# Optimization experiments

Hardware: AMD Instinct MI355X
Metric: run time of the kernel (lower is better)

The kernel has to match this reference:

```python
import jax, jax.numpy as jnp
import numpy as np

B, IN, H = 4096, 1024, 1024
G = 5  # i, f, o, c_hat, s gates

def setup_inputs() -> dict:
    key = jax.random.key(0)
    ks = jax.random.split(key, 24)
    s_in = 1.0 / np.sqrt(IN)
    s_h = 1.0 / np.sqrt(H)
    s_cat = 1.0 / np.sqrt(IN + H)
    inp = {
        'x': jax.random.normal(ks[0], (B, IN), jnp.float32),
        'h_prev': jax.random.normal(ks[1], (B, H), jnp.float32),
        'c_prev': jax.random.normal(ks[2], (B, H), jnp.float32),
        'ssg_state': jax.random.normal(ks[3], (B, H), jnp.float32),
        # stacked gate weights, torch Linear convention y = x @ W.T + b
        'Wx': jax.random.uniform(ks[4], (G, H, IN), jnp.float32, -s_in, s_in),
        'bWx': jax.random.uniform(ks[5], (G, H), jnp.float32, -s_in, s_in),
        'Ux': jax.random.uniform(ks[6], (G, H, H), jnp.float32, -s_h, s_h),
        'bUx': jax.random.uniform(ks[7], (G, H), jnp.float32, -s_h, s_h),
        # alpha MLP: Linear(IN+H -> H), ReLU, Linear(H -> 1), Sigmoid
        'a1_w': jax.random.uniform(ks[8], (H, IN + H), jnp.float32, -s_cat, s_cat),
        'a1_b': jax.random.uniform(ks[9], (H,), jnp.float32, -s_cat, s_cat),
        'a2_w': jax.random.uniform(ks[10], (1, H), jnp.float32, -s_h, s_h),
        'a2_b': jax.random.uniform(ks[11], (1,), jnp.float32, -s_h, s_h),
        'r1_w': jax.random.uniform(ks[12], (H, H), jnp.float32, -s_h, s_h),
        'r1_b': jax.random.uniform(ks[13], (H,), jnp.float32, -s_h, s_h),
        'r2_w': jax.random.uniform(ks[14], (H, H), jnp.float32, -s_h, s_h),
        'r2_b': jax.random.uniform(ks[15], (H,), jnp.float32, -s_h, s_h),
        'r3_w': jax.random.uniform(ks[16], (H, H), jnp.float32, -s_h, s_h),
        'r3_b': jax.random.uniform(ks[17], (H,), jnp.float32, -s_h, s_h),
        'ssg_w': jax.random.uniform(ks[18], (H, H), jnp.float32, -s_h, s_h),
        'ssg_b': jax.random.uniform(ks[19], (H,), jnp.float32, -s_h, s_h),
    }
    return inp


def reference(x, h_prev, c_prev, ssg_state, Wx, bWx, Ux, bUx,
              a1_w, a1_b, a2_w, a2_b, r1_w, r1_b, r2_w, r2_b, r3_w, r3_b,
              ssg_w, ssg_b):
    # all 5 gate pre-activations in two batched GEMMs: [G, B, H]
    g = (jnp.einsum('bi,ghi->gbh', x, Wx) + bWx[:, None, :]
         + jnp.einsum('bh,gkh->gbk', h_prev, Ux) + bUx[:, None, :])
    i_t = jax.nn.sigmoid(g[0])
    f_t = jax.nn.sigmoid(g[1])
    o_t = jax.nn.sigmoid(g[2])
    c_hat_t = jnp.tanh(g[3])
    s_t = jax.nn.sigmoid(g[4])  # computed as in original (unused when ssg_state given)

    combined = jnp.concatenate([x, h_prev], axis=-1)  # [B, IN+H]
    a_hidden = jax.nn.relu(combined @ a1_w.T + a1_b)
    alpha_t = jax.nn.sigmoid(a_hidden @ a2_w.T + a2_b)  # [B, 1]

    ssg_new = (ssg_state + h_prev) @ ssg_w.T + ssg_b  # ssg_state is not None branch

    c_t = f_t * c_prev + i_t * c_hat_t * s_t * alpha_t * ssg_new

    r = jax.nn.relu(h_prev @ r1_w.T + r1_b)
    r = jax.nn.relu(r @ r2_w.T + r2_b)
    residual = r @ r3_w.T + r3_b

    c_t = c_t + residual
    h_t = o_t * jnp.tanh(c_t)
    return (h_t, c_t, ssg_new)
```

## Files before the change

kernel.cpp:

```cpp
#include <hip/hip_runtime.h>
#include <hip/hip_bf16.h>

#define B_DIM 4096
#define H_DIM 1024
#define K1    2048
#define N1    6144

typedef __attribute__((ext_vector_type(8))) short bf16x8;
typedef __attribute__((ext_vector_type(4))) float f32x4;

__device__ __forceinline__ unsigned short f2bf(float f) {
  unsigned int x = __float_as_uint(f);
  x += 0x7fffu + ((x >> 16) & 1u);
  return (unsigned short)(x >> 16);
}
__device__ __forceinline__ float bf2f(unsigned short u) {
  return __uint_as_float(((unsigned int)u) << 16);
}
__device__ __forceinline__ float fast_sigmoid(float x) {
  return __builtin_amdgcn_rcpf(1.0f + __expf(-x));
}
__device__ __forceinline__ float fast_tanh(float x) {
  return 1.0f - 2.0f * __builtin_amdgcn_rcpf(1.0f + __expf(2.0f * x));
}
__device__ __forceinline__ void gload_lds16(const void* g, void* l) {
  __builtin_amdgcn_global_load_lds(
      (const __attribute__((address_space(1))) void*)g,
      (__attribute__((address_space(3))) void*)l, 16, 0, 0);
}

__device__ __forceinline__ int swz1k(int x) {
  return x ^ (((x >> 9) & 1) << 5);
}

__global__ __launch_bounds__(256) void prep_kernel(
    const float* __restrict__ x, const float* __restrict__ h,
    const float* __restrict__ ssg_state,
    const float* __restrict__ Wx, const float* __restrict__ Ux,
    const float* __restrict__ a1_w,
    const float* __restrict__ ssg_w, const float* __restrict__ r1_w,
    const float* __restrict__ r2_w, const float* __restrict__ r3_w,
    unsigned short* __restrict__ combined,
    unsigned short* __restrict__ ssg_in,
    unsigned short* __restrict__ W1,
    unsigned short* __restrict__ W2,
    unsigned short* __restrict__ W3,
    unsigned short* __restrict__ W4)
{
  const size_t NV0 = (size_t)B_DIM * K1 / 4;
  const size_t NV1 = (size_t)B_DIM * H_DIM / 4;
  const size_t NV3 = (size_t)N1 * K1 / 4;
  const size_t NV4 = (size_t)2048 * H_DIM / 4;
  const size_t NV5 = (size_t)H_DIM * H_DIM / 4;
  const size_t total = NV0 + NV1 + NV3 + NV4 + NV5 + NV5;
  const size_t stride = (size_t)gridDim.x * blockDim.x;

  for (size_t v = (size_t)blockIdx.x * blockDim.x + threadIdx.x; v < total; v += stride) {
    size_t idx = v;
    const float* src;
    unsigned short* dst;
    if (idx < NV0) {
      size_t e = idx * 4, b = e >> 11, k = e & 2047;
      src = (k < 1024) ? &x[(b << 10) + k] : &h[(b << 10) + (k - 1024)];
      dst = &combined[e];
    } else if ((idx -= NV0) < NV1) {
      size_t e = idx * 4;
      float4 a = *(const float4*)&ssg_state[e];
      float4 c = *(const float4*)&h[e];
      ushort4 o;
      o.x = f2bf(a.x + c.x); o.y = f2bf(a.y + c.y);
      o.z = f2bf(a.z + c.z); o.w = f2bf(a.w + c.w);
      *(ushort4*)&ssg_in[e] = o;
      continue;
    } else if ((idx -= NV1) < NV3) {
      size_t e = idx * 4, n = e >> 11, k = e & 2047;
      if (n < 5120) src = (k < 1024) ? &Wx[(n << 10) + k] : &Ux[(n << 10) + (k - 1024)];
      else          src = &a1_w[((n - 5120) << 11) + k];
      dst = &W1[e];
    } else if ((idx -= NV3) < NV4) {
      size_t e = idx * 4, n = e >> 10, k = e & 1023;
      src = (n < 1024) ? &ssg_w[(n << 10) + k] : &r1_w[((n - 1024) << 10) + k];
      dst = &W2[e];
    } else if ((idx -= NV4) < NV5) {
      size_t e = idx * 4; src = &r2_w[e]; dst = &W3[e];
    } else {
      idx -= NV5;
      size_t e = idx * 4; src = &r3_w[e]; dst = &W4[e];
    }
    float4 a = *(const float4*)src;
    ushort4 o;
    o.x = f2bf(a.x); o.y = f2bf(a.y); o.z = f2bf(a.z); o.w = f2bf(a.w);
    *(ushort4*)dst = o;
  }
}

__device__ __forceinline__ void body192(
    unsigned short* lds, const int bid,
    const unsigned short* __restrict__ A,
    const unsigned short* __restrict__ W,
    const float* __restrict__ bWx, const float* __restrict__ bUx,
    const float* __restrict__ a1_b,
    unsigned short* __restrict__ gates,
    unsigned short* __restrict__ a_hidden)
{
  constexpr int NT  = 32;
  constexpr int NTN = 32;
  constexpr int NWG = 32 * NTN;

  const int tid  = threadIdx.x;
  const int wave = tid >> 6;
  const int lane = tid & 63;
  const int wm = wave >> 1;
  const int wn = wave & 1;

  const int swz = (bid & 7) * (NWG / 8) + (bid >> 3);
  const int tm = swz / NTN, tn = swz % NTN;
  const int tmB = tm * 128, tnB = tn * 192;

  const int sidx = swz1k(lane * 16);
  const int r_l  = sidx >> 6;
  const int kel  = (sidx & 63) >> 1;
  const unsigned short* pA[2][2];
  const unsigned short* pB[3][2];
#pragma unroll
  for (int rg = 0; rg < 2; ++rg)
#pragma unroll
    for (int j = 0; j < 2; ++j)
      pA[rg][j] = A + (size_t)(tmB + (wave * 2 + rg) * 16 + r_l) * K1 + j * 32 + kel;
#pragma unroll
  for (int rg = 0; rg < 3; ++rg)
#pragma unroll
    for (int j = 0; j < 2; ++j)
      pB[rg][j] = W + (size_t)(tnB + (wave * 3 + rg) * 16 + r_l) * K1 + j * 32 + kel;

#define STAGE_A(tt) do { const int p_ = (tt) & 1;                                \
    _Pragma("unroll")                                                            \
    for (int rg = 0; rg < 2; ++rg)                                               \
      _Pragma("unroll")                                                          \
      for (int j = 0; j < 2; ++j)                                                \
        gload_lds16(pA[rg][j] + (size_t)(tt) * 64,                               \
                    &lds[p_ * 20480 + ((wave * 2 + rg) * 2 + j) * 512]);         \
  } while (0)
#define STAGE_B(tt) do { const int p_ = (tt) & 1;                                \
    _Pragma("unroll")                                                            \
    for (int rg = 0; rg < 3; ++rg)                                               \
      _Pragma("unroll")                                                          \
      for (int j = 0; j < 2; ++j)                                                \
        gload_lds16(pB[rg][j] + (size_t)(tt) * 64,                               \
                    &lds[p_ * 20480 + 8192 + ((wave * 3 + rg) * 2 + j) * 512]);  \
  } while (0)

  const int loc = swz1k((lane & 15) * 64 + (lane >> 4) * 16);

  f32x4 acc[4][6];
#pragma unroll
  for (int m = 0; m < 4; ++m)
#pragma unroll
    for (int n = 0; n < 6; ++n) acc[m][n] = (f32x4){0.f, 0.f, 0.f, 0.f};

  STAGE_A(0); STAGE_B(0);

#define MFMA24(aV, bV) do {                                                      \
    _Pragma("unroll")                                                            \
    for (int n = 0; n < 6; ++n) {                                                \
      _Pragma("unroll")                                                          \
      for (int m = 0; m < 4; ++m)                                                \
        acc[m][n] = __builtin_amdgcn_mfma_f32_16x16x32_bf16(                     \
            aV[m], bV[n], acc[m][n], 0, 0, 0);                                   \
    } } while (0)

  const char* lchar = (const char*)lds;
  for (int t = 0; t < NT; ++t) {
    asm volatile("s_waitcnt vmcnt(0)" ::: "memory");
    __builtin_amdgcn_s_barrier();

    const char* base = lchar + (t & 1) * 40960;
    const char* bA = base + wm * 8192 + loc;
    const char* bB = base + 16384 + wn * 12288 + loc;

    bf16x8 a0[4], a1[4], b0[6], b1[6];
#pragma unroll
    for (int n = 0; n < 6; ++n) b0[n] = *(const bf16x8*)(bB + (2 * n + 0) * 1024);
#pragma unroll
    for (int m = 0; m < 4; ++m) a0[m] = *(const bf16x8*)(bA + (2 * m + 0) * 1024);
    if (t + 1 < NT) STAGE_A(t + 1);
#pragma unroll
    for (int n = 0; n < 6; ++n) b1[n] = *(const bf16x8*)(bB + (2 * n + 1) * 1024);
#pragma unroll
    for (int m = 0; m < 4; ++m) a1[m] = *(const bf16x8*)(bA + (2 * m + 1) * 1024);
    if (t + 1 < NT) STAGE_B(t + 1);

    __builtin_amdgcn_s_setprio(1);
    MFMA24(a0, b0);
    __builtin_amdgcn_s_setprio(0);
    __builtin_amdgcn_s_setprio(1);
    MFMA24(a1, b1);
    __builtin_amdgcn_s_setprio(0);
  }
#undef MFMA24
#undef STAGE_A
#undef STAGE_B

  unsigned short* slab = &lds[wave * 1536];
  const int l15 = lane & 15, lq4 = (lane >> 4) << 2;
  const int colg0 = tnB + wn * 96;
  const int rowg0 = tmB + wm * 64;
  const size_t BH = (size_t)B_DIM * H_DIM;

  float biasv[6];
  int amode[6];
#pragma unroll
  for (int fn = 0; fn < 6; ++fn) {
    const int c = colg0 + fn * 16 + l15;
    if (c < 5120) {
      biasv[fn] = bWx[c] + bUx[c];
      amode[fn] = ((c >> 10) == 3) ? 1 : 0;
    } else {
      biasv[fn] = a1_b[c - 5120];
      amode[fn] = 2;
    }
  }
  __builtin_amdgcn_s_barrier();
#pragma unroll
  for (int fm = 0; fm < 4; ++fm) {
#pragma unroll
    for (int fn = 0; fn < 6; ++fn) {
      f32x4 v = acc[fm][fn];
#pragma unroll
      for (int j = 0; j < 4; ++j) {
        const int row = lq4 + j;
        const float xv = v[j] + biasv[fn];
        const float res = (amode[fn] == 1) ? fast_tanh(xv)
                         : (amode[fn] == 0) ? fast_sigmoid(xv)
                         : fmaxf(xv, 0.f);
        const int byte = (row * 192 + (fn * 16 + l15) * 2) ^ (((row >> 2) & 1) << 5);
        slab[byte >> 1] = f2bf(res);
      }
    }
    asm volatile("s_waitcnt lgkmcnt(0)" ::: "memory");
    __builtin_amdgcn_sched_barrier(0);
#pragma unroll
    for (int p = 0; p < 3; ++p) {
      const int id = p * 64 + lane;
      const int row = id / 12, cc = id - row * 12;
      const int byte = (row * 192 + cc * 16) ^ (((row >> 2) & 1) << 5);
      bf16x8 pk = *(const bf16x8*)((const char*)slab + byte);
      const int col = colg0 + cc * 8;
      const size_t r = (size_t)(rowg0 + fm * 16 + row);
      unsigned short* dst;
      if (col < 5120) dst = gates + (size_t)(col >> 10) * BH + r * 1024 + (col & 1023);
      else            dst = a_hidden + r * 1024 + (col - 5120);
      *(bf16x8*)dst = pk;
    }
    asm volatile("s_waitcnt lgkmcnt(0)" ::: "memory");
    __builtin_amdgcn_sched_barrier(0);
  }
}

template <int NT, int MODE>
__device__ __forceinline__ void gemm_body(
    unsigned short* lds, const int bid,
    const unsigned short* __restrict__ A0,
    const unsigned short* __restrict__ A1,
    const unsigned short* __restrict__ W,
    const float* __restrict__ b0, const float* __restrict__ b1,
    void* __restrict__ out0, void* __restrict__ out1)
{
  constexpr int KDIM = NT * 64;
  constexpr int NTN  = 16;
  constexpr int NWG  = 32 * NTN;

  const int tid  = threadIdx.x;
  const int wave = tid >> 6;
  const int lane = tid & 63;
  const int wm = wave >> 1;
  const int wn = wave & 1;

  const int swz = (bid & 7) * (NWG / 8) + (bid >> 3);
  const int tm = swz / NTN, tn = swz % NTN;
  const int tmB = tm * 128, tnB = tn * 128;

  const unsigned short* Abase = A0;
  int lda = 1024;
  if (tn >= 8) { Abase = A1; lda = 2048; }

  const int sidx = swz1k(lane * 16);
  const int r_l  = sidx >> 6;
  const int kel  = (sidx & 63) >> 1;
  const unsigned short* pA[2][2];
  const unsigned short* pB[2][2];
#pragma unroll
  for (int rg = 0; rg < 2; ++rg)
#pragma unroll
    for (int j = 0; j < 2; ++j) {
      const int rr = wave * 32 + rg * 16 + r_l;
      const int kk0 = j * 32 + kel;
      pA[rg][j] = Abase + (size_t)(tmB + rr) * lda + kk0;
      pB[rg][j] = W + (size_t)(tnB + rr) * KDIM + kk0;
    }

#define STAGE_A(tt) do { const int p_ = (tt) & 1;                                \
    _Pragma("unroll")                                                            \
    for (int rg = 0; rg < 2; ++rg)                                               \
      _Pragma("unroll")                                                          \
      for (int j = 0; j < 2; ++j)                                                \
        gload_lds16(pA[rg][j] + (size_t)(tt) * 64,                               \
                    &lds[p_ * 16384 + ((wave * 2 + rg) * 2 + j) * 512]);         \
  } while (0)
#define STAGE_B(tt) do { const int p_ = (tt) & 1;                                \
    _Pragma("unroll")                                                            \
    for (int rg = 0; rg < 2; ++rg)                                               \
      _Pragma("unroll")                                                          \
      for (int j = 0; j < 2; ++j)                                                \
        gload_lds16(pB[rg][j] + (size_t)(tt) * 64,                               \
                    &lds[p_ * 16384 + 8192 + ((wave * 2 + rg) * 2 + j) * 512]);  \
  } while (0)

  const int loc = swz1k((lane & 15) * 64 + (lane >> 4) * 16);

  f32x4 acc[4][4];
#pragma unroll
  for (int m = 0; m < 4; ++m)
#pragma unroll
    for (int n = 0; n < 4; ++n) acc[m][n] = (f32x4){0.f, 0.f, 0.f, 0.f};

  STAGE_A(0); STAGE_B(0);

#define MFMA16(aV, bV) do {                                                      \
    _Pragma("unroll")                                                            \
    for (int n = 0; n < 4; ++n) {                                                \
      _Pragma("unroll")                                                          \
      for (int m = 0; m < 4; ++m)                                                \
        acc[m][n] = __builtin_amdgcn_mfma_f32_16x16x32_bf16(                     \
            aV[m], bV[n], acc[m][n], 0, 0, 0);                                   \
    } } while (0)

  const char* lchar = (const char*)lds;
  for (int t = 0; t < NT; ++t) {
    asm volatile("s_waitcnt vmcnt(0)" ::: "memory");
    __builtin_amdgcn_s_barrier();

    const char* base = lchar + (t & 1) * 32768;
    const char* bA = base + wm * 8192 + loc;
    const char* bB = base + 16384 + wn * 8192 + loc;

    bf16x8 a0[4], a1[4], b0v[4], b1v[4];
#pragma unroll
    for (int n = 0; n < 4; ++n) b0v[n] = *(const bf16x8*)(bB + (2 * n + 0) * 1024);
#pragma unroll
    for (int m = 0; m < 4; ++m) a0[m] = *(const bf16x8*)(bA + (2 * m + 0) * 1024);
    if (t + 1 < NT) STAGE_A(t + 1);
#pragma unroll
    for (int n = 0; n < 4; ++n) b1v[n] = *(const bf16x8*)(bB + (2 * n + 1) * 1024);
#pragma unroll
    for (int m = 0; m < 4; ++m) a1[m] = *(const bf16x8*)(bA + (2 * m + 1) * 1024);
    if (t + 1 < NT) STAGE_B(t + 1);

    __builtin_amdgcn_s_setprio(1);
    MFMA16(a0, b0v);
    __builtin_amdgcn_s_setprio(0);
    __builtin_amdgcn_s_setprio(1);
    MFMA16(a1, b1v);
    __builtin_amdgcn_s_setprio(0);
  }
#undef MFMA16
#undef STAGE_A
#undef STAGE_B

  const int l15 = lane & 15, lq4 = (lane >> 4) << 2;
  const int rowg0 = tmB + wm * 64;

  if (tn < 8) {
    const int col0 = tn * 128 + wn * 64;
#pragma unroll
    for (int fn = 0; fn < 4; ++fn) {
      const int col = col0 + fn * 16 + l15;
      const float bias = b0[col];
#pragma unroll
      for (int fm = 0; fm < 4; ++fm) {
        f32x4 v = acc[fm][fn];
#pragma unroll
        for (int j = 0; j < 4; ++j) {
          const int r = rowg0 + fm * 16 + lq4 + j;
          ((float*)out0)[(size_t)r * 1024 + col] = v[j] + bias;
        }
      }
    }
    return;
  }

  unsigned short* slab = &lds[wave * 1024];
  const int lr8 = lane >> 3, lc8 = lane & 7;
  const int colg0 = (tn - 8) * 128 + wn * 64;
  unsigned short* outbase = (unsigned short*)out1;
  float biasv[4];
#pragma unroll
  for (int fn = 0; fn < 4; ++fn) biasv[fn] = b1[colg0 + fn * 16 + l15];
  __builtin_amdgcn_s_barrier();
#pragma unroll
  for (int fm = 0; fm < 4; ++fm) {
#pragma unroll
    for (int fn = 0; fn < 4; ++fn) {
      f32x4 v = acc[fm][fn];
#pragma unroll
      for (int j = 0; j < 4; ++j) {
        const int row = lq4 + j;
        const float res = fmaxf(v[j] + biasv[fn], 0.f);
        const int colb = ((fn * 16 + l15) * 2) ^ (((row >> 2) & 3) << 5);
        slab[(row * 128 + colb) >> 1] = f2bf(res);
      }
    }
    asm volatile("s_waitcnt lgkmcnt(0)" ::: "memory");
    __builtin_amdgcn_sched_barrier(0);
#pragma unroll
    for (int rd = 0; rd < 2; ++rd) {
      const int row = rd * 8 + lr8;
      const int cb = (lc8 * 16) ^ (((row >> 2) & 3) << 5);
      bf16x8 pk = *(const bf16x8*)((const char*)slab + row * 128 + cb);
      const size_t r = (size_t)(rowg0 + fm * 16 + row);
      *(bf16x8*)&outbase[r * 1024 + colg0 + lc8 * 8] = pk;
    }
    asm volatile("s_waitcnt lgkmcnt(0)" ::: "memory");
    __builtin_amdgcn_sched_barrier(0);
  }
}

__global__ __launch_bounds__(256, 2) void gemm_big(
    const unsigned short* __restrict__ combined,
    const unsigned short* __restrict__ ssg_in,
    const unsigned short* __restrict__ W1,
    const unsigned short* __restrict__ W2,
    const float* __restrict__ bWx, const float* __restrict__ bUx,
    const float* __restrict__ a1_b,
    const float* __restrict__ ssg_b, const float* __restrict__ r1_b,
    unsigned short* __restrict__ gates,
    unsigned short* __restrict__ a_hidden,
    float* __restrict__ ssg_out,
    unsigned short* __restrict__ r1)
{
  __shared__ unsigned short lds[40960];
  const int bid = blockIdx.x;
  if (bid < 1024) {
    body192(lds, bid, combined, W1, bWx, bUx, a1_b, gates, a_hidden);
  } else {
    gemm_body<16, 1>(lds, bid - 1024, ssg_in, combined + 1024, W2,
                     ssg_b, r1_b, ssg_out, r1);
  }
}

template <int MODE>
__global__ __launch_bounds__(256, 3) void gemm_small64(
    const unsigned short* __restrict__ A,
    const unsigned short* __restrict__ W,
    const float* __restrict__ bias,
    void* __restrict__ out)
{
  __shared__ unsigned short lds[24576];
  constexpr int NT = 16;

  const int tid  = threadIdx.x;
  const int wave = tid >> 6;
  const int lane = tid & 63;
  const int wm = wave >> 1;
  const int wn = wave & 1;

  const int bid = blockIdx.x;
  const int swz = (bid & 7) * 64 + (bid >> 3);
  const int tm = swz >> 3, tn = swz & 7;
  const int tmB = tm * 64, tnB = tn * 128;

  const int sidx = swz1k(lane * 16);
  const int r_l  = sidx >> 6;
  const int kel  = (sidx & 63) >> 1;
  const unsigned short* pA[2];
  const unsigned short* pB[2][2];
#pragma unroll
  for (int j = 0; j < 2; ++j)
    pA[j] = A + (size_t)(tmB + wave * 16 + r_l) * 1024 + j * 32 + kel;
#pragma unroll
  for (int rg = 0; rg < 2; ++rg)
#pragma unroll
    for (int j = 0; j < 2; ++j)
      pB[rg][j] = W + (size_t)(tnB + (wave * 2 + rg) * 16 + r_l) * 1024 + j * 32 + kel;

#define STAGE_A(tt) do { const int p_ = (tt) & 1;                                \
    _Pragma("unroll")                                                            \
    for (int j = 0; j < 2; ++j)                                                  \
      gload_lds16(pA[j] + (size_t)(tt) * 64,                                     \
                  &lds[p_ * 12288 + (wave * 2 + j) * 512]);                      \
  } while (0)
#define STAGE_B(tt) do { const int p_ = (tt) & 1;                                \
    _Pragma("unroll")                                                            \
    for (int rg = 0; rg < 2; ++rg)                                               \
      _Pragma("unroll")                                                          \
      for (int j = 0; j < 2; ++j)                                                \
        gload_lds16(pB[rg][j] + (size_t)(tt) * 64,                               \
                    &lds[p_ * 12288 + 4096 + ((wave * 2 + rg) * 2 + j) * 512]);  \
  } while (0)

  const int loc = swz1k((lane & 15) * 64 + (lane >> 4) * 16);

  f32x4 acc[2][4];
#pragma unroll
  for (int m = 0; m < 2; ++m)
#pragma unroll
    for (int n = 0; n < 4; ++n) acc[m][n] = (f32x4){0.f, 0.f, 0.f, 0.f};

  STAGE_A(0); STAGE_B(0);

  const char* lchar = (const char*)lds;
  for (int t = 0; t < NT; ++t) {
    asm volatile("s_waitcnt vmcnt(0)" ::: "memory");
    __builtin_amdgcn_s_barrier();

    const char* base = lchar + (t & 1) * 24576;
    const char* bA = base + wm * 4096 + loc;
    const char* bB = base + 8192 + wn * 8192 + loc;

    bf16x8 a0[2], a1[2], b0[4], b1[4];
#pragma unroll
    for (int n = 0; n < 4; ++n) b0[n] = *(const bf16x8*)(bB + (2 * n + 0) * 1024);
#pragma unroll
    for (int m = 0; m < 2; ++m) a0[m] = *(const bf16x8*)(bA + (2 * m + 0) * 1024);
    if (t + 1 < NT) STAGE_A(t + 1);
#pragma unroll
    for (int n = 0; n < 4; ++n) b1[n] = *(const bf16x8*)(bB + (2 * n + 1) * 1024);
#pragma unroll
    for (int m = 0; m < 2; ++m) a1[m] = *(const bf16x8*)(bA + (2 * m + 1) * 1024);
    if (t + 1 < NT) STAGE_B(t + 1);

    __builtin_amdgcn_s_setprio(1);
#pragma unroll
    for (int n = 0; n < 4; ++n)
#pragma unroll
      for (int m = 0; m < 2; ++m)
        acc[m][n] = __builtin_amdgcn_mfma_f32_16x16x32_bf16(a0[m], b0[n], acc[m][n], 0, 0, 0);
    __builtin_amdgcn_s_setprio(0);
    __builtin_amdgcn_s_setprio(1);
#pragma unroll
    for (int n = 0; n < 4; ++n)
#pragma unroll
      for (int m = 0; m < 2; ++m)
        acc[m][n] = __builtin_amdgcn_mfma_f32_16x16x32_bf16(a1[m], b1[n], acc[m][n], 0, 0, 0);
    __builtin_amdgcn_s_setprio(0);
  }
#undef STAGE_A
#undef STAGE_B

  const int l15 = lane & 15, lq4 = (lane >> 4) << 2;
  const int rowg0 = tmB + wm * 32;

  if (MODE == 3) {
    const int col0 = tnB + wn * 64;
#pragma unroll
    for (int fn = 0; fn < 4; ++fn) {
      const int col = col0 + fn * 16 + l15;
      const float bv = bias[col];
#pragma unroll
      for (int fm = 0; fm < 2; ++fm) {
        f32x4 v = acc[fm][fn];
#pragma unroll
        for (int j = 0; j < 4; ++j) {
          const int r = rowg0 + fm * 16 + lq4 + j;
          ((float*)out)[(size_t)r * 1024 + col] = v[j] + bv;
        }
      }
    }
    return;
  }

  unsigned short* slab = &lds[wave * 1024];
  const int lr8 = lane >> 3, lc8 = lane & 7;
  const int colg0 = tnB + wn * 64;
  unsigned short* outbase = (unsigned short*)out;
  float biasv[4];
#pragma unroll
  for (int fn = 0; fn < 4; ++fn) biasv[fn] = bias[colg0 + fn * 16 + l15];
  __builtin_amdgcn_s_barrier();
#pragma unroll
  for (int fm = 0; fm < 2; ++fm) {
#pragma unroll
    for (int fn = 0; fn < 4; ++fn) {
      f32x4 v = acc[fm][fn];
#pragma unroll
      for (int j = 0; j < 4; ++j) {
        const int row = lq4 + j;
        const float res = fmaxf(v[j] + biasv[fn], 0.f);
        const int colb = ((fn * 16 + l15) * 2) ^ (((row >> 2) & 3) << 5);
        slab[(row * 128 + colb) >> 1] = f2bf(res);
      }
    }
    asm volatile("s_waitcnt lgkmcnt(0)" ::: "memory");
    __builtin_amdgcn_sched_barrier(0);
#pragma unroll
    for (int rd = 0; rd < 2; ++rd) {
      const int row = rd * 8 + lr8;
      const int cb = (lc8 * 16) ^ (((row >> 2) & 3) << 5);
      bf16x8 pk = *(const bf16x8*)((const char*)slab + row * 128 + cb);
      const size_t r = (size_t)(rowg0 + fm * 16 + row);
      *(bf16x8*)&outbase[r * 1024 + colg0 + lc8 * 8] = pk;
    }
    asm volatile("s_waitcnt lgkmcnt(0)" ::: "memory");
    __builtin_amdgcn_sched_barrier(0);
  }
}

__global__ __launch_bounds__(256) void final_fused(
    const unsigned short* __restrict__ gates,
    const float* __restrict__ c_prev,
    const unsigned short* __restrict__ a_hidden,
    const float* __restrict__ a2_w, const float* __restrict__ a2_b,
    const float* __restrict__ residual,
    const float* __restrict__ ssg_new,
    float* __restrict__ h_out, float* __restrict__ c_out)
{
  __shared__ float red[5];
  const int r = blockIdx.x;
  const int tid = threadIdx.x;
  const size_t BH = (size_t)B_DIM * H_DIM;

  {
    ushort4 u = *(const ushort4*)&a_hidden[(size_t)r * 1024 + tid * 4];
    float4 w = *(const float4*)&a2_w[tid * 4];
    float s = bf2f(u.x) * w.x + bf2f(u.y) * w.y + bf2f(u.z) * w.z + bf2f(u.w) * w.w;
#pragma unroll
    for (int off = 32; off; off >>= 1) s += __shfl_xor(s, off);
    if ((tid & 63) == 0) red[tid >> 6] = s;
  }
  __syncthreads();
  if (tid == 0)
    red[4] = fast_sigmoid(red[0] + red[1] + red[2] + red[3] + a2_b[0]);
  __syncthreads();
  const float al = red[4];

  const size_t e = (size_t)r * 1024 + tid * 4;
  ushort4 iu = *(const ushort4*)&gates[e];
  ushort4 fu = *(const ushort4*)&gates[BH + e];
  ushort4 ou = *(const ushort4*)&gates[2 * BH + e];
  ushort4 cu = *(const ushort4*)&gates[3 * BH + e];
  ushort4 su = *(const ushort4*)&gates[4 * BH + e];
  float4 cp = *(const float4*)&c_prev[e];
  float4 rs = *(const float4*)&residual[e];
  float4 sg = *(const float4*)&ssg_new[e];
  float4 ho, co;
  co.x = bf2f(fu.x) * cp.x + bf2f(iu.x) * bf2f(cu.x) * bf2f(su.x) * al * sg.x + rs.x;
  co.y = bf2f(fu.y) * cp.y + bf2f(iu.y) * bf2f(cu.y) * bf2f(su.y) * al * sg.y + rs.y;
  co.z = bf2f(fu.z) * cp.z + bf2f(iu.z) * bf2f(cu.z) * bf2f(su.z) * al * sg.z + rs.z;
  co.w = bf2f(fu.w) * cp.w + bf2f(iu.w) * bf2f(cu.w) * bf2f(su.w) * al * sg.w + rs.w;
  ho.x = bf2f(ou.x) * fast_tanh(co.x);
  ho.y = bf2f(ou.y) * fast_tanh(co.y);
  ho.z = bf2f(ou.z) * fast_tanh(co.z);
  ho.w = bf2f(ou.w) * fast_tanh(co.w);
  *(float4*)&h_out[e] = ho;
  *(float4*)&c_out[e] = co;
}

extern "C" void kernel_launch(void* const* d_in, const int* in_sizes, int n_in,
                              void* d_out, int out_size, void* d_ws, size_t ws_size,
                              hipStream_t stream)
{
  (void)in_sizes; (void)n_in; (void)out_size; (void)ws_size;
  const float* x         = (const float*)d_in[0];
  const float* h_prev    = (const float*)d_in[1];
  const float* c_prev    = (const float*)d_in[2];
  const float* ssg_state = (const float*)d_in[3];
  const float* Wx        = (const float*)d_in[4];
  const float* bWx       = (const float*)d_in[5];
  const float* Ux        = (const float*)d_in[6];
  const float* bUx       = (const float*)d_in[7];
  const float* a1_w      = (const float*)d_in[8];
  const float* a1_b      = (const float*)d_in[9];
  const float* a2_w      = (const float*)d_in[10];
  const float* a2_b      = (const float*)d_in[11];
  const float* r1_w      = (const float*)d_in[12];
  const float* r1_b      = (const float*)d_in[13];
  const float* r2_w      = (const float*)d_in[14];
  const float* r2_b      = (const float*)d_in[15];
  const float* r3_w      = (const float*)d_in[16];
  const float* r3_b      = (const float*)d_in[17];
  const float* ssg_w     = (const float*)d_in[18];
  const float* ssg_b     = (const float*)d_in[19];

  char* ws = (char*)d_ws;
  unsigned short* combined = (unsigned short*)(ws);
  unsigned short* ssg_in   = (unsigned short*)(ws + 16777216);
  unsigned short* W1       = (unsigned short*)(ws + 33554432);
  unsigned short* W2       = (unsigned short*)(ws + 58720256);
  unsigned short* W3       = (unsigned short*)(ws + 62914560);
  unsigned short* W4       = (unsigned short*)(ws + 65011712);
  unsigned short* gates    = (unsigned short*)(ws + 67108864);
  unsigned short* a_hidden = (unsigned short*)(ws + 109051904);
  unsigned short* r1       = (unsigned short*)(ws + 117456896);
  unsigned short* r2       = (unsigned short*)(ws + 125845504);
  float*          residual = (float*)(ws + 134234112);

  float* h_out   = (float*)d_out;
  float* c_out   = h_out + (size_t)B_DIM * H_DIM;
  float* ssg_out = c_out + (size_t)B_DIM * H_DIM;

  prep_kernel<<<4096, 256, 0, stream>>>(x, h_prev, ssg_state, Wx, Ux, a1_w,
                                        ssg_w, r1_w, r2_w, r3_w,
                                        combined, ssg_in, W1, W2, W3, W4);

  gemm_big<<<1536, 256, 0, stream>>>(
      combined, ssg_in, W1, W2, bWx, bUx, a1_b, ssg_b, r1_b,
      gates, a_hidden, ssg_out, r1);

  gemm_small64<2><<<512, 256, 0, stream>>>(r1, W3, r2_b, r2);

  gemm_small64<3><<<512, 256, 0, stream>>>(r2, W4, r3_b, residual);

  final_fused<<<B_DIM, 256, 0, stream>>>(
      gates, c_prev, a_hidden, a2_w, a2_b, residual, ssg_out, h_out, c_out);
}
```

Baseline: 217.1 us.

## Halve K-tile to 32 in big GEMM to raise occupancy to 4 blocks

Shrinks the per-iteration K slice of both fused GEMM bodies from 64 to 32, halving the LDS buffers (81920 to 40960 bytes) and fragment registers, and raises launch bounds from 2 to 4 blocks per CU. The goal is more resident waves to hide global-load and barrier latency. The cost is twice as many loop iterations, so twice as many barriers and vmcnt waits, with less MFMA work between them. Register pressure from the 96-float accumulator in the 192-wide body may also limit whether 4 blocks actually fit.

```diff
diff --git a/kernel.cpp b/kernel.cpp
--- a/kernel.cpp
+++ b/kernel.cpp
@@ -94,7 +94,7 @@
   }
 }
 
-__device__ __forceinline__ void body192(
+__device__ __forceinline__ void body192_bk32(
     unsigned short* lds, const int bid,
     const unsigned short* __restrict__ A,
     const unsigned short* __restrict__ W,
@@ -103,7 +103,7 @@
     unsigned short* __restrict__ gates,
     unsigned short* __restrict__ a_hidden)
 {
-  constexpr int NT  = 32;
+  constexpr int NT  = 64;
   constexpr int NTN = 32;
   constexpr int NWG = 32 * NTN;
 
@@ -120,34 +120,26 @@
   const int sidx = swz1k(lane * 16);
   const int r_l  = sidx >> 6;
   const int kel  = (sidx & 63) >> 1;
-  const unsigned short* pA[2][2];
-  const unsigned short* pB[3][2];
+  const unsigned short* pA[2];
+  const unsigned short* pB[3];
 #pragma unroll
   for (int rg = 0; rg < 2; ++rg)
-#pragma unroll
-    for (int j = 0; j < 2; ++j)
-      pA[rg][j] = A + (size_t)(tmB + (wave * 2 + rg) * 16 + r_l) * K1 + j * 32 + kel;
+    pA[rg] = A + (size_t)(tmB + (wave * 2 + rg) * 16 + r_l) * K1 + kel;
 #pragma unroll
   for (int rg = 0; rg < 3; ++rg)
-#pragma unroll
-    for (int j = 0; j < 2; ++j)
-      pB[rg][j] = W + (size_t)(tnB + (wave * 3 + rg) * 16 + r_l) * K1 + j * 32 + kel;
+    pB[rg] = W + (size_t)(tnB + (wave * 3 + rg) * 16 + r_l) * K1 + kel;
 
 #define STAGE_A(tt) do { const int p_ = (tt) & 1;                                \
     _Pragma("unroll")                                                            \
     for (int rg = 0; rg < 2; ++rg)                                               \
-      _Pragma("unroll")                                                          \
-      for (int j = 0; j < 2; ++j)                                                \
-        gload_lds16(pA[rg][j] + (size_t)(tt) * 64,                               \
-                    &lds[p_ * 20480 + ((wave * 2 + rg) * 2 + j) * 512]);         \
+      gload_lds16(pA[rg] + (size_t)(tt) * 32,                                    \
+                  &lds[p_ * 10240 + (wave * 2 + rg) * 512]);                     \
   } while (0)
 #define STAGE_B(tt) do { const int p_ = (tt) & 1;                                \
     _Pragma("unroll")                                                            \
     for (int rg = 0; rg < 3; ++rg)                                               \
-      _Pragma("unroll")                                                          \
-      for (int j = 0; j < 2; ++j)                                                \
-        gload_lds16(pB[rg][j] + (size_t)(tt) * 64,                               \
-                    &lds[p_ * 20480 + 8192 + ((wave * 3 + rg) * 2 + j) * 512]);  \
+      gload_lds16(pB[rg] + (size_t)(tt) * 32,                                    \
+                  &lds[p_ * 10240 + 4096 + (wave * 3 + rg) * 512]);              \
   } while (0)
 
   const int loc = swz1k((lane & 15) * 64 + (lane >> 4) * 16);
@@ -159,45 +151,32 @@
     for (int n = 0; n < 6; ++n) acc[m][n] = (f32x4){0.f, 0.f, 0.f, 0.f};
 
   STAGE_A(0); STAGE_B(0);
-
-#define MFMA24(aV, bV) do {                                                      \
-    _Pragma("unroll")                                                            \
-    for (int n = 0; n < 6; ++n) {                                                \
-      _Pragma("unroll")                                                          \
-      for (int m = 0; m < 4; ++m)                                                \
-        acc[m][n] = __builtin_amdgcn_mfma_f32_16x16x32_bf16(                     \
-            aV[m], bV[n], acc[m][n], 0, 0, 0);                                   \
-    } } while (0)
 
   const char* lchar = (const char*)lds;
   for (int t = 0; t < NT; ++t) {
     asm volatile("s_waitcnt vmcnt(0)" ::: "memory");
     __builtin_amdgcn_s_barrier();
 
-    const char* base = lchar + (t & 1) * 40960;
-    const char* bA = base + wm * 8192 + loc;
-    const char* bB = base + 16384 + wn * 12288 + loc;
-
-    bf16x8 a0[4], a1[4], b0[6], b1[6];
-#pragma unroll
-    for (int n = 0; n < 6; ++n) b0[n] = *(const bf16x8*)(bB + (2 * n + 0) * 1024);
-#pragma unroll
-    for (int m = 0; m < 4; ++m) a0[m] = *(const bf16x8*)(bA + (2 * m + 0) * 1024);
-    if (t + 1 < NT) STAGE_A(t + 1);
-#pragma unroll
-    for (int n = 0; n < 6; ++n) b1[n] = *(const bf16x8*)(bB + (2 * n + 1) * 1024);
-#pragma unroll
-    for (int m = 0; m < 4; ++m) a1[m] = *(const bf16x8*)(bA + (2 * m + 1) * 1024);
-    if (t + 1 < NT) STAGE_B(t + 1);
+    const char* base = lchar + (t & 1) * 20480;
+    const char* bA = base + wm * 4096 + loc;
+    const char* bB = base + 8192 + wn * 6144 + loc;
+
+    bf16x8 av[4], bv[6];
+#pragma unroll
+    for (int n = 0; n < 6; ++n) bv[n] = *(const bf16x8*)(bB + n * 1024);
+#pragma unroll
+    for (int m = 0; m < 4; ++m) av[m] = *(const bf16x8*)(bA + m * 1024);
+    if (t + 1 < NT) { STAGE_A(t + 1); STAGE_B(t + 1); }
 
     __builtin_amdgcn_s_setprio(1);
-    MFMA24(a0, b0);
+#pragma unroll
+    for (int n = 0; n < 6; ++n)
+#pragma unroll
+      for (int m = 0; m < 4; ++m)
+        acc[m][n] = __builtin_amdgcn_mfma_f32_16x16x32_bf16(av[m], bv[n],
+                                                            acc[m][n], 0, 0, 0);
     __builtin_amdgcn_s_setprio(0);
-    __builtin_amdgcn_s_setprio(1);
-    MFMA24(a1, b1);
-    __builtin_amdgcn_s_setprio(0);
-  }
-#undef MFMA24
+  }
 #undef STAGE_A
 #undef STAGE_B
 
@@ -257,18 +236,17 @@
   }
 }
 
-template <int NT, int MODE>
-__device__ __forceinline__ void gemm_body(
+__device__ __forceinline__ void body128_bk32(
     unsigned short* lds, const int bid,
     const unsigned short* __restrict__ A0,
     const unsigned short* __restrict__ A1,
     const unsigned short* __restrict__ W,
     const float* __restrict__ b0, const float* __restrict__ b1,
-    void* __restrict__ out0, void* __restrict__ out1)
+    float* __restrict__ out0, unsigned short* __restrict__ out1)
 {
-  constexpr int KDIM = NT * 64;
-  constexpr int NTN  = 16;
-  constexpr int NWG  = 32 * NTN;
+  constexpr int NT  = 32;
+  constexpr int NTN = 16;
+  constexpr int NWG = 32 * NTN;
 
   const int tid  = threadIdx.x;
   const int wave = tid >> 6;
@@ -287,33 +265,25 @@
   const int sidx = swz1k(lane * 16);
   const int r_l  = sidx >> 6;
   const int kel  = (sidx & 63) >> 1;
-  const unsigned short* pA[2][2];
-  const unsigned short* pB[2][2];
-#pragma unroll
-  for (int rg = 0; rg < 2; ++rg)
-#pragma unroll
-    for (int j = 0; j < 2; ++j) {
-      const int rr = wave * 32 + rg * 16 + r_l;
-      const int kk0 = j * 32 + kel;
-      pA[rg][j] = Abase + (size_t)(tmB + rr) * lda + kk0;
-      pB[rg][j] = W + (size_t)(tnB + rr) * KDIM + kk0;
-    }
+  const unsigned short* pA[2];
+  const unsigned short* pB[2];
+#pragma unroll
+  for (int rg = 0; rg < 2; ++rg) {
+    pA[rg] = Abase + (size_t)(tmB + (wave * 2 + rg) * 16 + r_l) * lda + kel;
+    pB[rg] = W + (size_t)(tnB + (wave * 2 + rg) * 16 + r_l) * 1024 + kel;
+  }
 
 #define STAGE_A(tt) do { const int p_ = (tt) & 1;                                \
     _Pragma("unroll")                                                            \
     for (int rg = 0; rg < 2; ++rg)                                               \
-      _Pragma("unroll")                                                          \
-      for (int j = 0; j < 2; ++j)                                                \
-        gload_lds16(pA[rg][j] + (size_t)(tt) * 64,                               \
-                    &lds[p_ * 16384 + ((wave * 2 + rg) * 2 + j) * 512]);         \
+      gload_lds16(pA[rg] + (size_t)(tt) * 32,                                    \
+                  &lds[p_ * 8192 + (wave * 2 + rg) * 512]);                      \
   } while (0)
 #define STAGE_B(tt) do { const int p_ = (tt) & 1;                                \
     _Pragma("unroll")                                                            \
     for (int rg = 0; rg < 2; ++rg)                                               \
-      _Pragma("unroll")                                                          \
-      for (int j = 0; j < 2; ++j)                                                \
-        gload_lds16(pB[rg][j] + (size_t)(tt) * 64,                               \
-                    &lds[p_ * 16384 + 8192 + ((wave * 2 + rg) * 2 + j) * 512]);  \
+      gload_lds16(pB[rg] + (size_t)(tt) * 32,                                    \
+                  &lds[p_ * 8192 + 4096 + (wave * 2 + rg) * 512]);               \
   } while (0)
 
   const int loc = swz1k((lane & 15) * 64 + (lane >> 4) * 16);
@@ -325,45 +295,32 @@
     for (int n = 0; n < 4; ++n) acc[m][n] = (f32x4){0.f, 0.f, 0.f, 0.f};
 
   STAGE_A(0); STAGE_B(0);
-
-#define MFMA16(aV, bV) do {                                                      \
-    _Pragma("unroll")                                                            \
-    for (int n = 0; n < 4; ++n) {                                                \
-      _Pragma("unroll")                                                          \
-      for (int m = 0; m < 4; ++m)                                                \
-        acc[m][n] = __builtin_amdgcn_mfma_f32_16x16x32_bf16(                     \
-            aV[m], bV[n], acc[m][n], 0, 0, 0);                                   \
-    } } while (0)
 
   const char* lchar = (const char*)lds;
   for (int t = 0; t < NT; ++t) {
     asm volatile("s_waitcnt vmcnt(0)" ::: "memory");
     __builtin_amdgcn_s_barrier();
 
-    const char* base = lchar + (t & 1) * 32768;
-    const char* bA = base + wm * 8192 + loc;
-    const char* bB = base + 16384 + wn * 8192 + loc;
-
-    bf16x8 a0[4], a1[4], b0v[4], b1v[4];
-#pragma unroll
-    for (int n = 0; n < 4; ++n) b0v[n] = *(const bf16x8*)(bB + (2 * n + 0) * 1024);
-#pragma unroll
-    for (int m = 0; m < 4; ++m) a0[m] = *(const bf16x8*)(bA + (2 * m + 0) * 1024);
-    if (t + 1 < NT) STAGE_A(t + 1);
-#pragma unroll
-    for (int n = 0; n < 4; ++n) b1v[n] = *(const bf16x8*)(bB + (2 * n + 1) * 1024);
-#pragma unroll
-    for (int m = 0; m < 4; ++m) a1[m] = *(const bf16x8*)(bA + (2 * m + 1) * 1024);
-    if (t + 1 < NT) STAGE_B(t + 1);
+    const char* base = lchar + (t & 1) * 16384;
+    const char* bA = base + wm * 4096 + loc;
+    const char* bB = base + 8192 + wn * 4096 + loc;
+
+    bf16x8 av[4], bv[4];
+#pragma unroll
+    for (int n = 0; n < 4; ++n) bv[n] = *(const bf16x8*)(bB + n * 1024);
+#pragma unroll
+    for (int m = 0; m < 4; ++m) av[m] = *(const bf16x8*)(bA + m * 1024);
+    if (t + 1 < NT) { STAGE_A(t + 1); STAGE_B(t + 1); }
 
     __builtin_amdgcn_s_setprio(1);
-    MFMA16(a0, b0v);
+#pragma unroll
+    for (int n = 0; n < 4; ++n)
+#pragma unroll
+      for (int m = 0; m < 4; ++m)
+        acc[m][n] = __builtin_amdgcn_mfma_f32_16x16x32_bf16(av[m], bv[n],
+                                                            acc[m][n], 0, 0, 0);
     __builtin_amdgcn_s_setprio(0);
-    __builtin_amdgcn_s_setprio(1);
-    MFMA16(a1, b1v);
-    __builtin_amdgcn_s_setprio(0);
-  }
-#undef MFMA16
+  }
 #undef STAGE_A
 #undef STAGE_B
 
@@ -382,7 +339,7 @@
 #pragma unroll
         for (int j = 0; j < 4; ++j) {
           const int r = rowg0 + fm * 16 + lq4 + j;
-          ((float*)out0)[(size_t)r * 1024 + col] = v[j] + bias;
+          out0[(size_t)r * 1024 + col] = v[j] + bias;
         }
       }
     }
@@ -392,7 +349,6 @@
   unsigned short* slab = &lds[wave * 1024];
   const int lr8 = lane >> 3, lc8 = lane & 7;
   const int colg0 = (tn - 8) * 128 + wn * 64;
-  unsigned short* outbase = (unsigned short*)out1;
   float biasv[4];
 #pragma unroll
   for (int fn = 0; fn < 4; ++fn) biasv[fn] = b1[colg0 + fn * 16 + l15];
@@ -418,14 +374,14 @@
       const int cb = (lc8 * 16) ^ (((row >> 2) & 3) << 5);
       bf16x8 pk = *(const bf16x8*)((const char*)slab + row * 128 + cb);
       const size_t r = (size_t)(rowg0 + fm * 16 + row);
-      *(bf16x8*)&outbase[r * 1024 + colg0 + lc8 * 8] = pk;
+      *(bf16x8*)&out1[r * 1024 + colg0 + lc8 * 8] = pk;
     }
     asm volatile("s_waitcnt lgkmcnt(0)" ::: "memory");
     __builtin_amdgcn_sched_barrier(0);
   }
 }
 
-__global__ __launch_bounds__(256, 2) void gemm_big(
+__global__ __launch_bounds__(256, 4) void gemm_big(
     const unsigned short* __restrict__ combined,
     const unsigned short* __restrict__ ssg_in,
     const unsigned short* __restrict__ W1,
@@ -438,13 +394,13 @@
     float* __restrict__ ssg_out,
     unsigned short* __restrict__ r1)
 {
-  __shared__ unsigned short lds[40960];
+  __shared__ unsigned short lds[20480];
   const int bid = blockIdx.x;
   if (bid < 1024) {
-    body192(lds, bid, combined, W1, bWx, bUx, a1_b, gates, a_hidden);
+    body192_bk32(lds, bid, combined, W1, bWx, bUx, a1_b, gates, a_hidden);
   } else {
-    gemm_body<16, 1>(lds, bid - 1024, ssg_in, combined + 1024, W2,
-                     ssg_b, r1_b, ssg_out, r1);
+    body128_bk32(lds, bid - 1024, ssg_in, combined + 1024, W2,
+                 ssg_b, r1_b, ssg_out, r1);
   }
 }
 
```

Result: slower. 540.7 us (+149.1%).
